# Kernel optimization log

Measured on AMD Instinct MI355X. Metric: run time of the kernel, lower is better.

Reference implementation:

```python
import jax, jax.numpy as jnp
import numpy as np

N_POINTS = 2_000_000
GRID = 256  # voxel grid resolution (D=H=W), production-scale stand-in for source's 128


def setup_inputs() -> dict:
    key = jax.random.key(0)
    k1, k2, k3 = jax.random.split(key, 3)
    coords = jax.random.uniform(k1, (N_POINTS, 3), dtype=jnp.float32,
                                minval=-0.95, maxval=0.95)
    registration_pred = jax.random.normal(k2, (N_POINTS, 3), dtype=jnp.float32) * 0.02
    registration_gt = jax.random.normal(k3, (N_POINTS, 3), dtype=jnp.float32) * 0.02
    return {"registration_pred": registration_pred,
            "registration_gt": registration_gt,
            "coords": coords}


def _splat(pts, size):
    """Trilinear scatter (adjoint of F.grid_sample, align_corners=False,
    zero padding). pts: [N,3] normalized coords in (x,y,z) order mapping to
    (W,H,D). Splats weight 1 per point. Returns [D,H,W] volume."""
    D = H = W = size
    # grid_sample align_corners=False unnormalization: p = ((g+1)*size - 1)/2
    x = ((pts[:, 0] + 1.0) * W - 1.0) * 0.5
    y = ((pts[:, 1] + 1.0) * H - 1.0) * 0.5
    z = ((pts[:, 2] + 1.0) * D - 1.0) * 0.5
    x0f, y0f, z0f = jnp.floor(x), jnp.floor(y), jnp.floor(z)
    fx, fy, fz = x - x0f, y - y0f, z - z0f  # fractional offsets
    x0, y0, z0 = x0f.astype(jnp.int32), y0f.astype(jnp.int32), z0f.astype(jnp.int32)
    vol = jnp.zeros(D * H * W, dtype=pts.dtype)
    for dz in (0, 1):
        wz = fz if dz else (1.0 - fz)
        for dy in (0, 1):
            wy = fy if dy else (1.0 - fy)
            for dx in (0, 1):
                wx = fx if dx else (1.0 - fx)
                xi, yi, zi = x0 + dx, y0 + dy, z0 + dz
                valid = ((xi >= 0) & (xi < W) & (yi >= 0) & (yi < H)
                         & (zi >= 0) & (zi < D))
                w = jnp.where(valid, wx * wy * wz, 0.0)
                idx = jnp.where(valid, (zi * H + yi) * W + xi, 0)
                vol = vol.at[idx].add(w)
    return vol.reshape(D, H, W)


def reference(registration_pred, registration_gt, coords):
    pred_vol = _splat(coords + registration_pred, GRID)
    gt_vol = _splat(coords + registration_gt, GRID)
    # HuberLoss(reduction='sum', delta=1.0)
    d = pred_vol - gt_vol
    ad = jnp.abs(d)
    return jnp.sum(jnp.where(ad <= 1.0, 0.5 * d * d, ad - 0.5))
```

## Files before the change

### kernel.cpp

```cpp
#include <hip/hip_runtime.h>

#define GRID_RES 256
#define NCELLS 1024
#define NB 1024
#define BCAP 6144
#define NPT 2
#define ISEGCAP 5888

#define W_SCALE 2097152.0f
#define INV_W (1.0f / 2097152.0f)
#define L_SCALE 512.0f
#define INV_L (1.0f / 512.0f)

struct CEv { unsigned w0, w1q, xyz; };

__device__ __forceinline__ CEv make_cev(float px, float py, float pz,
                                        unsigned sign) {
    float x = ((px + 1.0f) * (float)GRID_RES - 1.0f) * 0.5f;
    float y = ((py + 1.0f) * (float)GRID_RES - 1.0f) * 0.5f;
    float z = ((pz + 1.0f) * (float)GRID_RES - 1.0f) * 0.5f;
    float xf = floorf(x), yf = floorf(y), zf = floorf(z);
    int x0 = (int)xf, y0 = (int)yf, z0 = (int)zf;
    unsigned qx = (unsigned)((x - xf) * 65535.0f + 0.5f);
    unsigned qy = (unsigned)((y - yf) * 65535.0f + 0.5f);
    unsigned qz = (unsigned)((z - zf) * 16383.0f + 0.5f);
    bool valid = (x0 >= -1) & (x0 <= 255) & (y0 >= -1) & (y0 <= 255) &
                 (z0 >= -1) & (z0 <= 255);
    CEv e;
    e.w0 = qx | (qy << 16);
    e.w1q = qz | (sign << 31);
    e.xyz = valid ? ((unsigned)(x0 + 1) | ((unsigned)(y0 + 1) << 10) |
                     ((unsigned)(z0 + 1) << 20) | (1u << 30))
                  : 0u;
    return e;
}

__device__ __forceinline__ bool ev_decode(const CEv& e, int& x0, int& y0,
                                          int& z0, int& xlo, int& xhi,
                                          int& ylo, int& yhi, int& zlo,
                                          int& zhi) {
    if (!(e.xyz & (1u << 30))) return false;
    x0 = (int)(e.xyz & 1023u) - 1;
    y0 = (int)((e.xyz >> 10) & 1023u) - 1;
    z0 = (int)((e.xyz >> 20) & 1023u) - 1;
    int cax = x0 >> 5, cbx = (x0 + 1) >> 5;
    xlo = (x0 >= 0) ? cax : cbx;
    xhi = (x0 <= 254) ? cbx : cax;
    int cay = y0 >> 5, cby = (y0 + 1) >> 5;
    ylo = (y0 >= 0) ? cay : cby;
    yhi = (y0 <= 254) ? cby : cay;
    int caz = z0 >> 4, cbz = (z0 + 1) >> 4;
    zlo = (z0 >= 0) ? caz : cbz;
    zhi = (z0 <= 254) ? cbz : caz;
    return true;
}

__global__ __launch_bounds__(1024) void bin_kernel(
    const float* __restrict__ pred, const float* __restrict__ gt,
    const float* __restrict__ coords, unsigned* __restrict__ segTab,
    uint2* __restrict__ payload, int* __restrict__ lossAcc,
    unsigned* __restrict__ doneCnt, int n) {
    __shared__ unsigned h[NCELLS];
    __shared__ unsigned wtot[16];
    __shared__ unsigned totalS;
    __shared__ uint4 plq[BCAP / 2];
    uint2* pl = (uint2*)plq;
    int b = blockIdx.x;
    int t = threadIdx.x;
    if (b == 0 && t == 0) {
        lossAcc[0] = 0;
        doneCnt[0] = 0;
    }
    h[t] = 0;
    __syncthreads();

    int chunk = (n + NB - 1) / NB;
    int start = b * chunk;
    int end = min(start + chunk, n);
    const float3* c3 = (const float3*)coords;
    const float3* p3 = (const float3*)pred;
    const float3* g3 = (const float3*)gt;

    CEv ev[2 * NPT];
#pragma unroll
    for (int k = 0; k < NPT; ++k) {
        int i = start + t + (k << 10);
        if (i < end) {
            float3 c = c3[i];
            float3 p = p3[i];
            float3 g = g3[i];
            ev[2 * k] = make_cev(c.x + p.x, c.y + p.y, c.z + p.z, 0u);
            ev[2 * k + 1] = make_cev(c.x + g.x, c.y + g.y, c.z + g.z, 1u);
        } else {
            ev[2 * k].xyz = 0;
            ev[2 * k + 1].xyz = 0;
        }
    }

#pragma unroll
    for (int k = 0; k < 2 * NPT; ++k) {
        int x0, y0, z0, xlo, xhi, ylo, yhi, zlo, zhi;
        if (ev_decode(ev[k], x0, y0, z0, xlo, xhi, ylo, yhi, zlo, zhi)) {
            for (int cz = zlo; cz <= zhi; ++cz)
                for (int cy = ylo; cy <= yhi; ++cy) {
                    int cyz = (cz << 6) | (cy << 3);
                    for (int cx = xlo; cx <= xhi; ++cx)
                        atomicAdd(&h[cyz | cx], 1u);
                }
        }
    }
    __syncthreads();

    unsigned x = h[t];
    unsigned incl = x;
    int lane = t & 63, wid = t >> 6;
#pragma unroll
    for (int off = 1; off < 64; off <<= 1) {
        unsigned y = __shfl_up(incl, off, 64);
        if (lane >= off) incl += y;
    }
    if (lane == 63) wtot[wid] = incl;
    __syncthreads();
    if (t == 0) {
        unsigned r = 0;
#pragma unroll
        for (int w = 0; w < 16; ++w) { unsigned v = wtot[w]; wtot[w] = r; r += v; }
        totalS = r;
    }
    __syncthreads();
    unsigned offE = incl - x + wtot[wid];
    segTab[(size_t)b * NCELLS + t] = (offE << 16) | x;
    h[t] = offE;
    __syncthreads();

#pragma unroll
    for (int k = 0; k < 2 * NPT; ++k) {
        int x0, y0, z0, xlo, xhi, ylo, yhi, zlo, zhi;
        if (ev_decode(ev[k], x0, y0, z0, xlo, xhi, ylo, yhi, zlo, zhi)) {
            unsigned w0 = ev[k].w0, w1q = ev[k].w1q;
            for (int cz = zlo; cz <= zhi; ++cz) {
                unsigned wz = w1q | ((unsigned)(z0 - (cz << 4) + 1) << 26);
                for (int cy = ylo; cy <= yhi; ++cy) {
                    unsigned wzy = wz | ((unsigned)(y0 - (cy << 5) + 1) << 20);
                    int cyz = (cz << 6) | (cy << 3);
                    for (int cx = xlo; cx <= xhi; ++cx) {
                        unsigned w1 =
                            wzy | ((unsigned)(x0 - (cx << 5) + 1) << 14);
                        unsigned slot = atomicAdd(&h[cyz | cx], 1u);
                        if (slot < (unsigned)BCAP) pl[slot] = make_uint2(w0, w1);
                    }
                }
            }
        }
    }
    __syncthreads();

    unsigned tot = totalS;
    unsigned m = min((tot + 1u) >> 1, (unsigned)(BCAP / 2));
    uint4* gp4 = (uint4*)(payload + (size_t)b * BCAP);
    for (unsigned i = t; i < m; i += 1024) gp4[i] = plq[i];
}

__device__ __forceinline__ void accum_item(uint2 p, int* v) {
    float fx = (float)(p.x & 0xFFFFu) * (1.0f / 65535.0f);
    float fy = (float)(p.x >> 16) * (1.0f / 65535.0f);
    float fz = (float)(p.y & 0x3FFFu) * (1.0f / 16383.0f);
    int lx = (int)((p.y >> 14) & 63u);
    int ly = (int)((p.y >> 20) & 63u);
    int lz = (int)((p.y >> 26) & 31u);
    float s = (p.y >> 31) ? -W_SCALE : W_SCALE;
    float wxs[2] = {1.0f - fx, fx};
    float wys[2] = {1.0f - fy, fy};
    float wzs[2] = {1.0f - fz, fz};
    int xb = lx - 1, yb = ly - 1, zb = lz - 1;
#pragma unroll
    for (int dz = 0; dz < 2; ++dz) {
        int rz = zb + dz;
        if ((unsigned)rz > 15u) continue;
        float wz = s * wzs[dz];
#pragma unroll
        for (int dy = 0; dy < 2; ++dy) {
            int ry = yb + dy;
            if ((unsigned)ry > 31u) continue;
            float wyz = wz * wys[dy];
#pragma unroll
            for (int dx = 0; dx < 2; ++dx) {
                int rx = xb + dx;
                if ((unsigned)rx > 31u) continue;
                int iw = __float2int_rn(wyz * wxs[dx]);
                atomicAdd(&v[(rz << 10) | (ry << 5) | rx], iw);
            }
        }
    }
}

__global__ __launch_bounds__(1024) void accum_kernel(
    const uint2* __restrict__ payload, const unsigned* __restrict__ segTab,
    int* __restrict__ lossAcc, unsigned* __restrict__ doneCnt,
    float* __restrict__ out) {
    __shared__ int4 v4s[4096];
    __shared__ unsigned short itemSeg[ISEGCAP];
    __shared__ unsigned pbs[NB];
    __shared__ unsigned w16[16];
    __shared__ float wsum[16];
    __shared__ unsigned totalS;
    int* v = (int*)v4s;
    int c = blockIdx.x;
    int t = threadIdx.x;
    unsigned tab = segTab[(size_t)t * NCELLS + c];
    int4 z; z.x = 0; z.y = 0; z.z = 0; z.w = 0;
#pragma unroll
    for (int j = 0; j < 4; ++j) v4s[t + (j << 10)] = z;

    unsigned cnt = tab & 0xFFFFu;
    unsigned off = tab >> 16;
    int lane = t & 63, wid = t >> 6;
    unsigned incl = cnt;
#pragma unroll
    for (int o = 1; o < 64; o <<= 1) {
        unsigned y = __shfl_up(incl, o, 64);
        if (lane >= o) incl += y;
    }
    if (lane == 63) w16[wid] = incl;
    __syncthreads();
    if (t == 0) {
        unsigned r = 0;
#pragma unroll
        for (int w = 0; w < 16; ++w) { unsigned q = w16[w]; w16[w] = r; r += q; }
        totalS = r;
    }
    __syncthreads();
    unsigned base = incl - cnt + w16[wid];
    pbs[t] = (unsigned)t * (unsigned)BCAP + off - base;
    for (unsigned k = 0; k < cnt; ++k) {
        unsigned idx = base + k;
        if (idx < (unsigned)ISEGCAP) itemSeg[idx] = (unsigned short)t;
    }
    __syncthreads();

    unsigned total = min(totalS, (unsigned)ISEGCAP);
    unsigned i0 = (unsigned)t, i1 = i0 + 1024, i2 = i0 + 2048, i3 = i0 + 3072,
             i4 = i0 + 4096, i5 = i0 + 5120;
    bool b0 = i0 < total, b1 = i1 < total, b2 = i2 < total, b3 = i3 < total,
         b4 = i4 < total, b5 = i5 < total;
    uint2 p0 = make_uint2(0, 0), p1 = p0, p2 = p0, p3 = p0, p4 = p0, p5 = p0;
    if (b0) p0 = payload[(size_t)(unsigned)(pbs[itemSeg[i0]] + i0)];
    if (b1) p1 = payload[(size_t)(unsigned)(pbs[itemSeg[i1]] + i1)];
    if (b2) p2 = payload[(size_t)(unsigned)(pbs[itemSeg[i2]] + i2)];
    if (b3) p3 = payload[(size_t)(unsigned)(pbs[itemSeg[i3]] + i3)];
    if (b4) p4 = payload[(size_t)(unsigned)(pbs[itemSeg[i4]] + i4)];
    if (b5) p5 = payload[(size_t)(unsigned)(pbs[itemSeg[i5]] + i5)];
    if (b0) accum_item(p0, v);
    if (b1) accum_item(p1, v);
    if (b2) accum_item(p2, v);
    if (b3) accum_item(p3, v);
    if (b4) accum_item(p4, v);
    if (b5) accum_item(p5, v);
    __syncthreads();

    float acc = 0.0f;
#pragma unroll
    for (int j = 0; j < 4; ++j) {
        int4 q = v4s[t + (j << 10)];
        {
            float d = (float)q.x * INV_W;
            float ad = fabsf(d);
            acc += (ad <= 1.0f) ? 0.5f * d * d : ad - 0.5f;
        }
        {
            float d = (float)q.y * INV_W;
            float ad = fabsf(d);
            acc += (ad <= 1.0f) ? 0.5f * d * d : ad - 0.5f;
        }
        {
            float d = (float)q.z * INV_W;
            float ad = fabsf(d);
            acc += (ad <= 1.0f) ? 0.5f * d * d : ad - 0.5f;
        }
        {
            float d = (float)q.w * INV_W;
            float ad = fabsf(d);
            acc += (ad <= 1.0f) ? 0.5f * d * d : ad - 0.5f;
        }
    }
#pragma unroll
    for (int o = 32; o > 0; o >>= 1) acc += __shfl_down(acc, o, 64);
    if (lane == 0) wsum[wid] = acc;
    __syncthreads();
    if (t == 0) {
        float tsum = 0.0f;
#pragma unroll
        for (int w = 0; w < 16; ++w) tsum += wsum[w];
        atomicAdd(lossAcc, __float2int_rn(tsum * L_SCALE));
        __threadfence();
        unsigned done = atomicAdd(doneCnt, 1u);
        if (done == (unsigned)(NCELLS - 1)) {
            __threadfence();
            int lv = atomicAdd(lossAcc, 0);
            out[0] = (float)lv * INV_L;
        }
    }
}

extern "C" void kernel_launch(void* const* d_in, const int* in_sizes, int n_in,
                              void* d_out, int out_size, void* d_ws, size_t ws_size,
                              hipStream_t stream) {
    const float* reg_pred = (const float*)d_in[0];
    const float* reg_gt   = (const float*)d_in[1];
    const float* coords   = (const float*)d_in[2];
    float* out = (float*)d_out;

    char* ws = (char*)d_ws;
    int* lossAcc = (int*)ws;
    unsigned* doneCnt = (unsigned*)(ws + 64);
    unsigned* segTab = (unsigned*)(ws + 256);
    uint2* payload = (uint2*)(ws + 256 + (size_t)NB * NCELLS * 4);

    int n = in_sizes[0] / 3;

    bin_kernel<<<NB, 1024, 0, stream>>>(reg_pred, reg_gt, coords, segTab,
                                        payload, lossAcc, doneCnt, n);
    accum_kernel<<<NCELLS, 1024, 0, stream>>>(payload, segTab, lossAcc,
                                              doneCnt, out);
}
```

Before: 178.6 us.

## Scatter binned payload into per-cell global regions via atomic cursors

Each bin block now reserves space in a per-cell global region with an atomic cursor and scatters its items straight into cell-contiguous payload storage. This replaces the per-block segment table and the per-cell gather that needed a prefix scan and segment map. The accumulate kernel then streams one contiguous region per cell with vectorized loads. In exchange it adds a small init kernel, global atomics and scattered 8-byte global writes, and the global order of items within a cell is no longer deterministic.

```diff
diff --git a/kernel.cpp b/kernel.cpp
--- a/kernel.cpp
+++ b/kernel.cpp
@@ -4,8 +4,8 @@
 #define NCELLS 1024
 #define NB 1024
 #define BCAP 6144
+#define CCAP 6144
 #define NPT 2
-#define ISEGCAP 5888
 
 #define W_SCALE 2097152.0f
 #define INV_W (1.0f / 2097152.0f)
@@ -55,22 +55,26 @@
     return true;
 }
 
+__global__ void init_kernel(unsigned* __restrict__ gCursor,
+                            int* __restrict__ lossAcc,
+                            unsigned* __restrict__ doneCnt) {
+    int t = threadIdx.x;
+    gCursor[t] = 0;
+    if (t == 0) { lossAcc[0] = 0; doneCnt[0] = 0; }
+}
+
 __global__ __launch_bounds__(1024) void bin_kernel(
     const float* __restrict__ pred, const float* __restrict__ gt,
-    const float* __restrict__ coords, unsigned* __restrict__ segTab,
-    uint2* __restrict__ payload, int* __restrict__ lossAcc,
-    unsigned* __restrict__ doneCnt, int n) {
+    const float* __restrict__ coords, unsigned* __restrict__ gCursor,
+    uint2* __restrict__ payload, int n) {
     __shared__ unsigned h[NCELLS];
+    __shared__ unsigned gAdj[NCELLS];
+    __shared__ unsigned short itemCell[BCAP];
     __shared__ unsigned wtot[16];
     __shared__ unsigned totalS;
-    __shared__ uint4 plq[BCAP / 2];
-    uint2* pl = (uint2*)plq;
+    __shared__ uint2 pl[BCAP];
     int b = blockIdx.x;
     int t = threadIdx.x;
-    if (b == 0 && t == 0) {
-        lossAcc[0] = 0;
-        doneCnt[0] = 0;
-    }
     h[t] = 0;
     __syncthreads();
 
@@ -129,8 +133,10 @@
     }
     __syncthreads();
     unsigned offE = incl - x + wtot[wid];
-    segTab[(size_t)b * NCELLS + t] = (offE << 16) | x;
     h[t] = offE;
+
+    unsigned gdst = atomicAdd(&gCursor[t], x);
+    gAdj[t] = (unsigned)t * (unsigned)CCAP + gdst - offE;
     __syncthreads();
 
 #pragma unroll
@@ -146,8 +152,12 @@
                     for (int cx = xlo; cx <= xhi; ++cx) {
                         unsigned w1 =
                             wzy | ((unsigned)(x0 - (cx << 5) + 1) << 14);
-                        unsigned slot = atomicAdd(&h[cyz | cx], 1u);
-                        if (slot < (unsigned)BCAP) pl[slot] = make_uint2(w0, w1);
+                        int cell = cyz | cx;
+                        unsigned slot = atomicAdd(&h[cell], 1u);
+                        if (slot < (unsigned)BCAP) {
+                            pl[slot] = make_uint2(w0, w1);
+                            itemCell[slot] = (unsigned short)cell;
+                        }
                     }
                 }
             }
@@ -155,10 +165,12 @@
     }
     __syncthreads();
 
-    unsigned tot = totalS;
-    unsigned m = min((tot + 1u) >> 1, (unsigned)(BCAP / 2));
-    uint4* gp4 = (uint4*)(payload + (size_t)b * BCAP);
-    for (unsigned i = t; i < m; i += 1024) gp4[i] = plq[i];
+    unsigned tot = min(totalS, (unsigned)BCAP);
+    for (unsigned i = t; i < tot; i += 1024) {
+        unsigned cell = itemCell[i];
+        unsigned d = gAdj[cell] + i;
+        if (d < (cell + 1u) * (unsigned)CCAP) payload[d] = pl[i];
+    }
 }
 
 __device__ __forceinline__ void accum_item(uint2 p, int* v) {
@@ -195,69 +207,36 @@
 }
 
 __global__ __launch_bounds__(1024) void accum_kernel(
-    const uint2* __restrict__ payload, const unsigned* __restrict__ segTab,
+    const uint2* __restrict__ payload, const unsigned* __restrict__ gCursor,
     int* __restrict__ lossAcc, unsigned* __restrict__ doneCnt,
     float* __restrict__ out) {
     __shared__ int4 v4s[4096];
-    __shared__ unsigned short itemSeg[ISEGCAP];
-    __shared__ unsigned pbs[NB];
-    __shared__ unsigned w16[16];
     __shared__ float wsum[16];
-    __shared__ unsigned totalS;
+    __shared__ unsigned cntS;
     int* v = (int*)v4s;
     int c = blockIdx.x;
     int t = threadIdx.x;
-    unsigned tab = segTab[(size_t)t * NCELLS + c];
+    if (t == 0) cntS = gCursor[c];
     int4 z; z.x = 0; z.y = 0; z.z = 0; z.w = 0;
 #pragma unroll
     for (int j = 0; j < 4; ++j) v4s[t + (j << 10)] = z;
-
-    unsigned cnt = tab & 0xFFFFu;
-    unsigned off = tab >> 16;
+    __syncthreads();
+
+    unsigned cnt = min(cntS, (unsigned)CCAP);
+    const uint4* p4 = (const uint4*)(payload + (size_t)c * CCAP);
+    unsigned n2 = cnt >> 1;
+    for (unsigned i = t; i < n2; i += 1024) {
+        uint4 q = p4[i];
+        uint2 pa; pa.x = q.x; pa.y = q.y;
+        uint2 pb; pb.x = q.z; pb.y = q.w;
+        accum_item(pa, v);
+        accum_item(pb, v);
+    }
+    if ((cnt & 1u) && t == 0)
+        accum_item(payload[(size_t)c * CCAP + cnt - 1], v);
+    __syncthreads();
+
     int lane = t & 63, wid = t >> 6;
-    unsigned incl = cnt;
-#pragma unroll
-    for (int o = 1; o < 64; o <<= 1) {
-        unsigned y = __shfl_up(incl, o, 64);
-        if (lane >= o) incl += y;
-    }
-    if (lane == 63) w16[wid] = incl;
-    __syncthreads();
-    if (t == 0) {
-        unsigned r = 0;
-#pragma unroll
-        for (int w = 0; w < 16; ++w) { unsigned q = w16[w]; w16[w] = r; r += q; }
-        totalS = r;
-    }
-    __syncthreads();
-    unsigned base = incl - cnt + w16[wid];
-    pbs[t] = (unsigned)t * (unsigned)BCAP + off - base;
-    for (unsigned k = 0; k < cnt; ++k) {
-        unsigned idx = base + k;
-        if (idx < (unsigned)ISEGCAP) itemSeg[idx] = (unsigned short)t;
-    }
-    __syncthreads();
-
-    unsigned total = min(totalS, (unsigned)ISEGCAP);
-    unsigned i0 = (unsigned)t, i1 = i0 + 1024, i2 = i0 + 2048, i3 = i0 + 3072,
-             i4 = i0 + 4096, i5 = i0 + 5120;
-    bool b0 = i0 < total, b1 = i1 < total, b2 = i2 < total, b3 = i3 < total,
-         b4 = i4 < total, b5 = i5 < total;
-    uint2 p0 = make_uint2(0, 0), p1 = p0, p2 = p0, p3 = p0, p4 = p0, p5 = p0;
-    if (b0) p0 = payload[(size_t)(unsigned)(pbs[itemSeg[i0]] + i0)];
-    if (b1) p1 = payload[(size_t)(unsigned)(pbs[itemSeg[i1]] + i1)];
-    if (b2) p2 = payload[(size_t)(unsigned)(pbs[itemSeg[i2]] + i2)];
-    if (b3) p3 = payload[(size_t)(unsigned)(pbs[itemSeg[i3]] + i3)];
-    if (b4) p4 = payload[(size_t)(unsigned)(pbs[itemSeg[i4]] + i4)];
-    if (b5) p5 = payload[(size_t)(unsigned)(pbs[itemSeg[i5]] + i5)];
-    if (b0) accum_item(p0, v);
-    if (b1) accum_item(p1, v);
-    if (b2) accum_item(p2, v);
-    if (b3) accum_item(p3, v);
-    if (b4) accum_item(p4, v);
-    if (b5) accum_item(p5, v);
-    __syncthreads();
-
     float acc = 0.0f;
 #pragma unroll
     for (int j = 0; j < 4; ++j) {
@@ -313,13 +292,14 @@
     char* ws = (char*)d_ws;
     int* lossAcc = (int*)ws;
     unsigned* doneCnt = (unsigned*)(ws + 64);
-    unsigned* segTab = (unsigned*)(ws + 256);
-    uint2* payload = (uint2*)(ws + 256 + (size_t)NB * NCELLS * 4);
+    unsigned* gCursor = (unsigned*)(ws + 256);
+    uint2* payload = (uint2*)(ws + 256 + 4096);
 
     int n = in_sizes[0] / 3;
 
-    bin_kernel<<<NB, 1024, 0, stream>>>(reg_pred, reg_gt, coords, segTab,
-                                        payload, lossAcc, doneCnt, n);
-    accum_kernel<<<NCELLS, 1024, 0, stream>>>(payload, segTab, lossAcc,
+    init_kernel<<<1, 1024, 0, stream>>>(gCursor, lossAcc, doneCnt);
+    bin_kernel<<<NB, 1024, 0, stream>>>(reg_pred, reg_gt, coords, gCursor,
+                                        payload, n);
+    accum_kernel<<<NCELLS, 1024, 0, stream>>>(payload, gCursor, lossAcc,
                                               doneCnt, out);
 }
```

Result: faster. 165.7 us (-7.2%).
